# Kernel optimization log

Measured on AMD Instinct MI355X. Metric: run time of the kernel, lower is better.

## Reference

```python
import jax, jax.numpy as jnp
import numpy as np

HEADS, DIM_HEAD, DIM = 12, 64, 768
H = W = 32
N = H * W
B = 4


def _ln(x, g, b, eps=1e-5):
    mu = x.mean(-1, keepdims=True)
    var = ((x - mu) ** 2).mean(-1, keepdims=True)
    return (x - mu) / jnp.sqrt(var + eps) * g + b


def _get_epipolar(k, src_c2w, target_c2w, h=H, w=W):
    # Faithful port of Epipolar_Attention.get_epipolar, without the (hw*hw,3) repeat
    # materialization (uses broadcasting for the pairwise cross product instead).
    b = k.shape[0]
    Wf = h * 16.0 / 9.0
    k = k.astype(jnp.float32)
    k = k.at[:, 0, :].multiply(Wf).at[:, 1, :].multiply(float(h))
    k = k.at[:, 0, 2].set(h / 2.0).at[:, 1, 2].set(h / 2.0)
    ii, jj = jnp.meshgrid(jnp.arange(h), jnp.arange(w), indexing='ij')
    # after the torch column swap: (col, row, 1)
    coords = jnp.stack([jj.ravel(), ii.ravel(), jnp.ones(h * w, jnp.int32)], axis=1).astype(jnp.float32)  # [hw,3]
    k3 = k[:, :3, :3]
    src_r, src_t = src_c2w[:, :3, :3].astype(jnp.float32), src_c2w[:, :3, 3].astype(jnp.float32)
    tgt_r, tgt_t = target_c2w[:, :3, :3].astype(jnp.float32), target_c2w[:, :3, 3].astype(jnp.float32)
    tgt_rinv = jnp.linalg.inv(tgt_r)
    fx, fy = k3[:, 0, 0][:, None], k3[:, 1, 1][:, None]
    cx, cy = k3[:, 0, 2][:, None], k3[:, 1, 2][:, None]
    nc = jnp.stack([(coords[None, :, 0] - cx) / fx,
                    (coords[None, :, 1] - cy) / fy,
                    jnp.broadcast_to(coords[None, :, 2], (b, h * w))], axis=-1)  # [b,hw,3]
    p3w = jnp.einsum('bij,bnj->bni', src_r, nc) + src_t[:, None]
    p2 = jnp.einsum('bij,bnj->bni', tgt_rinv, p3w) - tgt_t[:, None]  # target_w2c_t = -target_c2w_t
    pij_un = jnp.einsum('bij,bnj->bni', k3, p2)                      # [b,hw,3]
    pij = pij_un / (pij_un[..., -1:] + 1e-6)
    o2 = jnp.einsum('bij,bj->bi', tgt_rinv, src_t) - tgt_t           # origin projected
    oij = jnp.einsum('bij,bj->bi', k3, o2)
    oij = oij / oij[..., -1:]
    oi_to_pi = pij - oij[:, None]                # [b,hw,3]
    oi_to_coord = coords[None] - oij[:, None]    # [b,hw,3]
    cr = jnp.cross(oi_to_pi[:, :, None, :], oi_to_coord[:, None, :, :])  # [b,hw,hw,3]
    area = jnp.sqrt((cr * cr).sum(-1))
    vlen = jnp.sqrt((oi_to_pi * oi_to_pi).sum(-1))[:, :, None]
    dist = area / vlen
    dw = 1.0 - jax.nn.sigmoid(50.0 * (dist - 0.5))
    row_max = dw.max(-1, keepdims=True)
    return jnp.where(row_max < 0.5, 1.0, dw)     # rows with max<0.5 are set to all-ones


def setup_inputs():
    key = jax.random.key(0)
    ks = jax.random.split(key, 16)
    s = 0.02
    x = jax.random.normal(ks[0], (B, N, DIM), jnp.float32)
    src_encode = jax.random.normal(ks[1], (B, N, DIM), jnp.float32)
    intrinsic = (jnp.zeros((B, 4, 4), jnp.float32)
                 .at[:, 0, 0].set(1.0).at[:, 1, 1].set(1.0)
                 .at[:, 0, 2].set(0.5).at[:, 1, 2].set(0.5)
                 .at[:, 2, 2].set(1.0).at[:, 3, 3].set(1.0))
    R = jnp.eye(3, dtype=jnp.float32) + 0.1 * jax.random.normal(ks[2], (2, B, 3, 3), jnp.float32)
    t = 0.5 * jax.random.normal(ks[3], (2, B, 3), jnp.float32)
    c2w = (jnp.zeros((2, B, 4, 4), jnp.float32)
           .at[:, :, :3, :3].set(R).at[:, :, :3, 3].set(t).at[:, :, 3, 3].set(1.0))
    hd = HEADS * DIM_HEAD
    w_ = lambda k_, shp: s * jax.random.normal(k_, shp, jnp.float32)
    return dict(
        x=x, src_encode=src_encode, intrinsic=intrinsic, c2w=c2w,
        lnq_g=jnp.ones(DIM), lnq_b=jnp.zeros(DIM), Wq=w_(ks[4], (DIM, hd)), bq=jnp.zeros(hd),
        lnk_g=jnp.ones(DIM), lnk_b=jnp.zeros(DIM), Wk=w_(ks[5], (DIM, hd)), bk=jnp.zeros(hd),
        lnv_g=jnp.ones(DIM), lnv_b=jnp.zeros(DIM), Wv=w_(ks[6], (DIM, hd)), bv=jnp.zeros(hd),
        Wp=w_(ks[7], (hd, DIM)), bp=jnp.zeros(DIM),
        pre_g=jnp.ones(DIM), pre_b=jnp.zeros(DIM),
        W1=w_(ks[8], (DIM, 2 * DIM)), b1=jnp.zeros(2 * DIM),
        W2=w_(ks[9], (2 * DIM, DIM)), b2=jnp.zeros(DIM),
        post_g=jnp.ones(DIM), post_b=jnp.zeros(DIM))


def reference(x, src_encode, intrinsic, c2w, lnq_g, lnq_b, Wq, bq, lnk_g, lnk_b, Wk, bk,
              lnv_g, lnv_b, Wv, bv, Wp, bp, pre_g, pre_b, W1, b1, W2, b2, post_g, post_b):
    b, n, _ = x.shape
    scale = DIM_HEAD ** -0.5
    split = lambda t_: t_.reshape(b, n, HEADS, DIM_HEAD).transpose(0, 2, 1, 3)  # [b,m,n,d]
    q = split(_ln(x, lnq_g, lnq_b) @ Wq + bq)
    k = split(_ln(src_encode, lnk_g, lnk_b) @ Wk + bk)
    v = split(_ln(src_encode, lnv_g, lnv_b) @ Wv + bv)
    scores = scale * jnp.einsum('bmqd,bmkd->bmqk', q, k)
    e1 = _get_epipolar(intrinsic, c2w[1], c2w[0])                    # do_epipolar
    e2 = jnp.swapaxes(_get_epipolar(intrinsic, c2w[0], c2w[1]), 1, 2)  # bidirectional (transposed)
    wmap = e1 * e2                                                   # [b,n,n], shared across heads
    att = jax.nn.softmax(scores * wmap[:, None], axis=-1)
    a = jnp.einsum('bmqk,bmkd->bmqd', att, v).transpose(0, 2, 1, 3).reshape(b, n, HEADS * DIM_HEAD)
    z = _ln(a @ Wp + bp, pre_g, pre_b)
    z = z + (jax.nn.gelu(z @ W1 + b1, approximate=False) @ W2 + b2)  # torch nn.GELU = exact erf
    z = _ln(z, post_g, post_b)
    wm_full = jnp.broadcast_to(wmap[:, None], (b, HEADS, n, n)).reshape(b * HEADS, n, n)
    return z, wm_full
```

## Files before the change

kernel.cpp:

```cpp
#include <hip/hip_runtime.h>
#include <hip/hip_bf16.h>

typedef unsigned short u16;
typedef __attribute__((ext_vector_type(4))) unsigned short u16x4;
typedef __attribute__((ext_vector_type(8))) unsigned short u16x8;
typedef __attribute__((ext_vector_type(8))) short s16x8;
typedef __attribute__((ext_vector_type(4))) float f32x4;

#define HEADS 12
#define NSEQ 1024
#define DIMM 768
#define DHEAD 64

__device__ __forceinline__ float b2f(u16 h) {
  union { unsigned u; float f; } v; v.u = ((unsigned)h) << 16; return v.f;
}
__device__ __forceinline__ u16 f2b(float f) {
  union { float f; unsigned u; } v; v.f = f;
  unsigned r = v.u + 0x7fffu + ((v.u >> 16) & 1u);
  return (u16)(r >> 16);
}
__device__ __forceinline__ void gl_lds16(const u16* g, u16* l) {
  __builtin_amdgcn_global_load_lds(
      (const __attribute__((address_space(1))) void*)g,
      (__attribute__((address_space(3))) void*)l, 16, 0, 0);
}

template<bool GELU, bool RESID, bool VTOUT>
__device__ __forceinline__ void gemm64(
    const u16* __restrict__ A, const u16* __restrict__ BT,
    const float* __restrict__ bias, const u16* __restrict__ resid,
    const float* __restrict__ rg, const float* __restrict__ rb,
    u16* __restrict__ C, int K, int lda, int ldb, int ldc,
    int m0, int n0, u16* As, u16* Bs, u16* __restrict__ vt)
{
  const int tid = threadIdx.x;
  const int lane = tid & 63;
  const int wv = tid >> 6;
  const int wm0 = (wv >> 1) * 32;
  const int wn0 = (wv & 1) * 32;
  const int l15 = lane & 15;
  const int quad = lane >> 4;
  const int srow = wv * 8 + (lane >> 3);
  const int schunk = lane & 7;
  const int scol = (schunk ^ (srow & 7)) * 8;

  f32x4 acc[2][2];
  #pragma unroll
  for (int i = 0; i < 2; ++i)
    #pragma unroll
    for (int j = 0; j < 2; ++j)
      acc[i][j] = {0.f, 0.f, 0.f, 0.f};

  const u16* Ab = A + (long)(m0 + srow) * lda + scol;
  const u16* Bb = BT + (long)(n0 + srow) * ldb + scol;

  auto issue = [&](int buf, int kk) {
    #pragma unroll
    for (int s = 0; s < 2; ++s) {
      gl_lds16(Ab + kk + (long)s * 32 * lda, As + buf * 4096 + s * 2048 + wv * 512);
      gl_lds16(Bb + kk + (long)s * 32 * ldb, Bs + buf * 4096 + s * 2048 + wv * 512);
    }
  };

  const int NK = K >> 6;
  issue(0, 0);
  issue(1, 64);

  int cur = 0;
  for (int i = 0; i < NK; ++i) {
    if (i + 1 < NK) asm volatile("s_waitcnt vmcnt(4)" ::: "memory");
    else            asm volatile("s_waitcnt vmcnt(0)" ::: "memory");
    __builtin_amdgcn_s_barrier();
    __builtin_amdgcn_sched_barrier(0);
    if (i + 2 < NK) {
      int nb = cur + 2; if (nb >= 3) nb -= 3;
      issue(nb, (i + 2) * 64);
    }
    const u16* Ac = As + cur * 4096;
    const u16* Bc = Bs + cur * 4096;
    #pragma unroll
    for (int kk = 0; kk < 2; ++kk) {
      s16x8 af[2], bfr[2];
      #pragma unroll
      for (int i2 = 0; i2 < 2; ++i2)
        af[i2] = *(const s16x8*)&Ac[(wm0 + i2 * 16 + l15) * 64 +
                                    (((kk * 4 + quad) ^ (l15 & 7)) * 8)];
      #pragma unroll
      for (int j = 0; j < 2; ++j)
        bfr[j] = *(const s16x8*)&Bc[(wn0 + j * 16 + l15) * 64 +
                                    (((kk * 4 + quad) ^ (l15 & 7)) * 8)];
      #pragma unroll
      for (int i2 = 0; i2 < 2; ++i2)
        #pragma unroll
        for (int j = 0; j < 2; ++j)
          acc[i2][j] = __builtin_amdgcn_mfma_f32_16x16x32_bf16(af[i2], bfr[j], acc[i2][j], 0, 0, 0);
    }
    ++cur; if (cur == 3) cur = 0;
  }

  if (VTOUT) {
    __syncthreads();
    u16* shp = As;
    const int b = m0 >> 10;
    const int nloc = m0 & 1023;
    const int fb0 = n0 - 768;
    #pragma unroll
    for (int j = 0; j < 2; ++j) {
      const float bvv = bias[n0 + wn0 + j * 16 + l15];
      #pragma unroll
      for (int i = 0; i < 2; ++i)
        #pragma unroll
        for (int v = 0; v < 4; ++v)
          shp[(wm0 + i * 16 + quad * 4 + v) * 72 + (wn0 + j * 16 + l15)] =
              f2b(acc[i][j][v] + bvv);
    }
    __syncthreads();
    const int f = tid >> 2;
    const int nb = (tid & 3) * 16;
    u16x8 o0, o1;
    #pragma unroll
    for (int nn = 0; nn < 8; ++nn) {
      o0[nn] = shp[(nb + nn) * 72 + f];
      o1[nn] = shp[(nb + 8 + nn) * 72 + f];
    }
    u16* dst = vt + ((long)(b * 768 + fb0 + f)) * NSEQ + nloc + nb;
    *(u16x8*)&dst[0] = o0;
    *(u16x8*)&dst[8] = o1;
    return;
  }

  #pragma unroll
  for (int i = 0; i < 2; ++i)
    #pragma unroll
    for (int j = 0; j < 2; ++j) {
      const int col = n0 + wn0 + j * 16 + l15;
      const float bvv = bias[col];
      #pragma unroll
      for (int v = 0; v < 4; ++v) {
        const int row = m0 + wm0 + i * 16 + quad * 4 + v;
        float val = acc[i][j][v] + bvv;
        if (GELU) val = 0.5f * val * (1.0f + erff(val * 0.70710678118654752440f));
        if (RESID) val += b2f(resid[(long)row * ldc + col]) * rg[col] + rb[col];
        C[(long)row * ldc + col] = f2b(val);
      }
    }
}

template<bool GELU, bool RESID>
__global__ __launch_bounds__(256)
void gemm_one(const u16* __restrict__ A, const u16* __restrict__ BT,
              const float* __restrict__ bias, const u16* __restrict__ resid,
              const float* __restrict__ rg, const float* __restrict__ rb,
              u16* __restrict__ C, int K, int lda, int ldb, int ldc)
{
  __shared__ u16 As[12288], Bs[12288];
  gemm64<GELU, RESID, false>(A, BT, bias, resid, rg, rb, C, K, lda, ldb, ldc,
                             blockIdx.x * 64, blockIdx.y * 64, As, Bs, nullptr);
}

__device__ __forceinline__ float dwval(f32x4 U, float ox, float oy, float oz, int m)
{
  const float cx = (float)(m & 31) - ox;
  const float cy = (float)(m >> 5) - oy;
  const float cz = 1.0f - oz;
  const float crx = U.y * cz - U.z * cy;
  const float cry = U.z * cx - U.x * cz;
  const float crz = U.x * cy - U.y * cx;
  const float area = sqrtf(crx * crx + cry * cry + crz * crz);
  const float dist = area / U.w;
  const float t = 50.0f * (dist - 0.5f);
  return 1.0f - 1.0f / (1.0f + __expf(-t));
}

#define PREP_T0 13824
#define PREP_T1 14016
#define PREP_T2 22208
#define PREP_T3 30400

__global__ __launch_bounds__(256)
void prep2(const float* w0, const float* w1, const float* w2,
           const float* w3, const float* w4, const float* w5,
           const float* gq, const float* gk, const float* gv, const float* gp,
           u16* d0, u16* d12, u16* d3, u16* d4, u16* d5,
           const float* bq, const float* bk, const float* bv, const float* b1,
           const float* lnqb, const float* lnkb, const float* lnvb, const float* preb,
           float* obq, float* obkv, float* ob1,
           const float* intr, const float* c2w,
           float* u4, float* oijb, float* flags,
           const float* nx, const float* nsrc, u16* onx, u16* onsrc)
{
  const int bid = blockIdx.x;
  const int tid = threadIdx.x;

  if (bid < PREP_T0) {
    __shared__ u16 t[32][36];
    const int z = bid / 2304;
    const int rem = bid - z * 2304;
    const int bx = rem % 48, by = rem / 48;
    const float* src; const float* g; u16* dst; int R, C; float sc = 1.0f;
    switch (z) {
      case 0: src = w0; g = gq; dst = d0;  R = 768;  C = 768;  sc = 0.125f; break;
      case 1: src = w1; g = gk; dst = d12; R = 768;  C = 768;  break;
      case 2: src = w2; g = gv; dst = d12 + 768 * 768; R = 768; C = 768; break;
      case 3: src = w3; g = nullptr; dst = d3; R = 768;  C = 768;  break;
      case 4: src = w4; g = gp; dst = d4; R = 768;  C = 1536; break;
      default: src = w5; g = nullptr; dst = d5; R = 1536; C = 768; break;
    }
    const int c0 = bx * 32;
    const int r0 = by * 32;
    if (c0 >= C || r0 >= R) return;
    const int i = tid >> 3;
    const int j4 = (tid & 7) * 4;
    const float rs = (g ? g[r0 + i] : 1.0f) * sc;
    #pragma unroll
    for (int jj = 0; jj < 4; ++jj)
      t[i][j4 + jj] = f2b(src[(long)(r0 + i) * C + c0 + j4 + jj] * rs);
    __syncthreads();
    u16x4 ov;
    #pragma unroll
    for (int jj = 0; jj < 4; ++jj) ov[jj] = t[j4 + jj][i];
    *(u16x4*)&dst[(long)(c0 + i) * R + r0 + j4] = ov;
    return;
  }

  if (bid < PREP_T1) {
    __shared__ float red[8][32];
    const int idx = bid - PREP_T0;
    const int y = idx / 48;
    const int bx = idx % 48;
    const float* W; const float* bln; const float* bw; float* out;
    int C; float sc = 1.0f;
    switch (y) {
      case 0: W = w0; bln = lnqb; bw = bq; out = obq;        C = 768;  sc = 0.125f; break;
      case 1: W = w1; bln = lnkb; bw = bk; out = obkv;       C = 768;  break;
      case 2: W = w2; bln = lnvb; bw = bv; out = obkv + 768; C = 768;  break;
      default: W = w4; bln = preb; bw = b1; out = ob1;       C = 1536; break;
    }
    const int c0 = bx * 32;
    if (c0 >= C) return;
    const int cl = tid & 31;
    const int rg = tid >> 5;
    const int c = c0 + cl;
    float s = 0.f;
    for (int r = rg * 96; r < rg * 96 + 96; ++r)
      s += bln[r] * W[(long)r * C + c];
    red[rg][cl] = s;
    __syncthreads();
    if (rg == 0) {
      float tot = bw[c];
      #pragma unroll
      for (int k = 0; k < 8; ++k) tot += red[k][cl];
      out[c] = tot * sc;
    }
    return;
  }

  if (bid < PREP_T2) {
    __shared__ float S[40];
    __shared__ float redf[8];
    const int rowid = bid - PREP_T1;
    const int db = rowid >> 10;
    const int n = rowid & 1023;
    const int d = db >> 2, b = db & 3;
    if (tid == 0) {
      const int sidx = (d == 0) ? 1 : 0;
      const int tidx = 1 - sidx;
      float k3[9], sr[9], st[3], tr[9], tt[3];
      const float Wf = 32.0f * 16.0f / 9.0f;
      for (int j = 0; j < 3; ++j) {
        k3[j]     = intr[(b * 4 + 0) * 4 + j] * Wf;
        k3[3 + j] = intr[(b * 4 + 1) * 4 + j] * 32.0f;
        k3[6 + j] = intr[(b * 4 + 2) * 4 + j];
      }
      k3[2] = 16.0f; k3[5] = 16.0f;
      for (int i = 0; i < 3; ++i) {
        for (int j = 0; j < 3; ++j) {
          sr[i * 3 + j] = c2w[((sidx * 4 + b) * 4 + i) * 4 + j];
          tr[i * 3 + j] = c2w[((tidx * 4 + b) * 4 + i) * 4 + j];
        }
        st[i] = c2w[((sidx * 4 + b) * 4 + i) * 4 + 3];
        tt[i] = c2w[((tidx * 4 + b) * 4 + i) * 4 + 3];
      }
      double a = tr[0], bb_ = tr[1], c = tr[2];
      double dd2 = tr[3], e = tr[4], f = tr[5];
      double g2 = tr[6], h2 = tr[7], i2 = tr[8];
      double det = a * (e * i2 - f * h2) - bb_ * (dd2 * i2 - f * g2) + c * (dd2 * h2 - e * g2);
      double inv[9] = {
        (e * i2 - f * h2), (c * h2 - bb_ * i2), (bb_ * f - c * e),
        (f * g2 - dd2 * i2), (a * i2 - c * g2), (c * dd2 - a * f),
        (dd2 * h2 - e * g2), (bb_ * g2 - a * h2), (a * e - bb_ * dd2)
      };
      float tri[9];
      for (int t2 = 0; t2 < 9; ++t2) tri[t2] = (float)(inv[t2] / det);
      float o2[3], oij[3];
      for (int i3 = 0; i3 < 3; ++i3)
        o2[i3] = tri[i3 * 3] * st[0] + tri[i3 * 3 + 1] * st[1] + tri[i3 * 3 + 2] * st[2] - tt[i3];
      for (int i3 = 0; i3 < 3; ++i3)
        oij[i3] = k3[i3 * 3] * o2[0] + k3[i3 * 3 + 1] * o2[1] + k3[i3 * 3 + 2] * o2[2];
      const float ozf = oij[2];
      oij[0] = oij[0] / ozf; oij[1] = oij[1] / ozf; oij[2] = ozf / ozf;
      if (n == 0) {
        oijb[db * 4 + 0] = oij[0]; oijb[db * 4 + 1] = oij[1];
        oijb[db * 4 + 2] = oij[2]; oijb[db * 4 + 3] = 0.f;
      }
      const float ncx = ((float)(n & 31) - k3[2]) / k3[0];
      const float ncy = ((float)(n >> 5) - k3[5]) / k3[4];
      const float p0 = sr[0] * ncx + sr[1] * ncy + sr[2] + st[0];
      const float p1 = sr[3] * ncx + sr[4] * ncy + sr[5] + st[1];
      const float p2 = sr[6] * ncx + sr[7] * ncy + sr[8] + st[2];
      const float q0 = tri[0] * p0 + tri[1] * p1 + tri[2] * p2 - tt[0];
      const float q1 = tri[3] * p0 + tri[4] * p1 + tri[5] * p2 - tt[1];
      const float q2 = tri[6] * p0 + tri[7] * p1 + tri[8] * p2 - tt[2];
      const float ww0 = k3[0] * q0 + k3[1] * q1 + k3[2] * q2;
      const float ww1 = k3[3] * q0 + k3[4] * q1 + k3[5] * q2;
      const float ww2 = k3[6] * q0 + k3[7] * q1 + k3[8] * q2;
      const float pz = ww2 + 1e-6f;
      const float ux = ww0 / pz - oij[0];
      const float uy = ww1 / pz - oij[1];
      const float uz = ww2 / pz - oij[2];
      const float vlen = sqrtf(ux * ux + uy * uy + uz * uz);
      f32x4 uo = {ux, uy, uz, vlen};
      *(f32x4*)&u4[(long)rowid * 4] = uo;
      S[33] = oij[0]; S[34] = oij[1]; S[35] = oij[2];
      S[36] = ux; S[37] = uy; S[38] = uz; S[39] = vlen;
    }
    __syncthreads();
    const f32x4 U = {S[36], S[37], S[38], S[39]};
    const float ox = S[33], oy = S[34], oz = S[35];
    float mx = -1e30f;
    #pragma unroll
    for (int i = 0; i < 4; ++i)
      mx = fmaxf(mx, dwval(U, ox, oy, oz, tid + i * 256));
    #pragma unroll
    for (int off = 32; off; off >>= 1) mx = fmaxf(mx, __shfl_down(mx, off));
    const int lane = tid & 63, wid = tid >> 6;
    if (!lane) redf[wid] = mx;
    __syncthreads();
    if (!tid) {
      const float m4 = fmaxf(fmaxf(redf[0], redf[1]), fmaxf(redf[2], redf[3]));
      flags[rowid] = (m4 < 0.5f) ? 1.0f : 0.0f;
    }
    return;
  }

  {
    __shared__ float s1[8], s2[8];
    const int r = bid - PREP_T2;
    const float* p = ((r < 4096) ? nx : nsrc) + (long)(r & 4095) * DIMM;
    u16* o = ((r < 4096) ? onx : onsrc) + (long)(r & 4095) * DIMM;
    float v0 = p[tid], v1 = p[tid + 256], v2 = p[tid + 512];
    float s = v0 + v1 + v2;
    #pragma unroll
    for (int off = 32; off; off >>= 1) s += __shfl_down(s, off);
    const int lane = tid & 63, wid = tid >> 6;
    if (!lane) s1[wid] = s;
    __syncthreads();
    if (!tid) s1[4] = s1[0] + s1[1] + s1[2] + s1[3];
    __syncthreads();
    const float mu = s1[4] / 768.0f;
    float d0 = v0 - mu, d1 = v1 - mu, d2 = v2 - mu;
    float sq = d0 * d0 + d1 * d1 + d2 * d2;
    #pragma unroll
    for (int off = 32; off; off >>= 1) sq += __shfl_down(sq, off);
    if (!lane) s2[wid] = sq;
    __syncthreads();
    if (!tid) s2[4] = s2[0] + s2[1] + s2[2] + s2[3];
    __syncthreads();
    const float rstd = 1.0f / sqrtf(s2[4] / 768.0f + 1e-5f);
    o[tid]       = f2b(d0 * rstd);
    o[tid + 256] = f2b(d1 * rstd);
    o[tid + 512] = f2b(d2 * rstd);
  }
}

__global__ __launch_bounds__(256)
void stageB(const u16* __restrict__ nx, const u16* __restrict__ ns,
            const u16* __restrict__ qT, const u16* __restrict__ kvT,
            const float* __restrict__ bqf, const float* __restrict__ bkvf,
            u16* __restrict__ qb, u16* __restrict__ kvb, u16* __restrict__ vT,
            const float* __restrict__ u4, const float* __restrict__ oijb,
            const float* __restrict__ flags,
            u16* __restrict__ wm, float* __restrict__ wm_full)
{
  __shared__ __align__(16) u16 sh[24576];
  const int bid = blockIdx.x;
  const int tid = threadIdx.x;

  if (bid < 2304) {
    u16* As = sh;
    u16* Bs = sh + 12288;
    const int z = bid / 768;
    const int idx = bid - z * 768;
    const int x = idx & 63;
    const int y = idx >> 6;
    if (z == 0)
      gemm64<false, false, false>(nx, qT, bqf, nullptr, nullptr, nullptr, qb,
                                  768, 768, 768, 768,
                                  x * 64, y * 64, As, Bs, nullptr);
    else if (z == 1)
      gemm64<false, false, false>(ns, kvT, bkvf, nullptr, nullptr, nullptr, kvb,
                                  768, 768, 768, 1536,
                                  x * 64, y * 64, As, Bs, nullptr);
    else
      gemm64<false, false, true>(ns, kvT, bkvf, nullptr, nullptr, nullptr, nullptr,
                                 768, 768, 768, 1536,
                                 x * 64, 768 + y * 64, As, Bs, vT);
    return;
  }

  const int id = bid - 2304;
  const int qx = id & 31;
  const int ky = (id >> 5) & 31;
  const int b = id >> 10;
  const int q0 = qx * 32;
  const int k0 = ky * 32;
  const int i = tid >> 3;
  const int j4 = (tid & 7) * 4;

  f32x4* U2s = (f32x4*)sh;
  float* f2s = (float*)(sh + 256);
  float* f1s = (float*)(sh + 320);
  if (tid < 32) {
    U2s[tid] = *(const f32x4*)&u4[((long)(4 + b) * 1024 + k0 + tid) * 4];
    f2s[tid] = flags[(4 + b) * 1024 + k0 + tid];
    f1s[tid] = flags[b * 1024 + q0 + tid];
  }
  __syncthreads();

  const int q = q0 + i;
  const f32x4 U1 = *(const f32x4*)&u4[((long)b * 1024 + q) * 4];
  const float o1x = oijb[b * 4 + 0], o1y = oijb[b * 4 + 1], o1z = oijb[b * 4 + 2];
  const float o2x = oijb[(4 + b) * 4 + 0], o2y = oijb[(4 + b) * 4 + 1], o2z = oijb[(4 + b) * 4 + 2];
  const bool fl1 = f1s[i] > 0.5f;

  u16x4 pk;
  f32x4 wf;
  #pragma unroll
  for (int jj = 0; jj < 4; ++jj) {
    const int k = k0 + j4 + jj;
    const float e1 = fl1 ? 1.0f : dwval(U1, o1x, o1y, o1z, k);
    const float e2 = (f2s[j4 + jj] > 0.5f) ? 1.0f : dwval(U2s[j4 + jj], o2x, o2y, o2z, q);
    const float w = e1 * e2;
    wf[jj] = w;
    pk[jj] = f2b(w);
  }
  *(u16x4*)&wm[((long)b * 1024 + q0 + i) * 1024 + k0 + j4] = pk;
  #pragma unroll
  for (int h = 0; h < HEADS; ++h)
    *(f32x4*)&wm_full[((long)(b * HEADS + h) * 1024 + q0 + i) * 1024 + k0 + j4] = wf;
}

__global__ __launch_bounds__(256, 3)
void fattn(const u16* __restrict__ qb, const u16* __restrict__ kvb,
           const u16* __restrict__ vT, const u16* __restrict__ wm,
           u16* __restrict__ outA)
{
  __shared__ u16 Qs[2 * 64 * 32];
  __shared__ u16 Ks[2][2 * 64 * 32];
  __shared__ u16 Vs[2][2 * 64 * 32];
  __shared__ u16 Ps[64][72];

  const int bh = blockIdx.y;
  const int b = bh / HEADS, h = bh - b * HEADS;
  const int q0 = blockIdx.x * 64;
  const int tid = threadIdx.x;
  const int lane = tid & 63;
  const int wv = tid >> 6;
  const int l15 = lane & 15;
  const int quad = lane >> 4;
  const int srow = lane >> 2;
  const int sscol = ((lane & 3) ^ (srow & 3)) * 8;
  const int rch = (quad ^ (l15 & 3)) * 8;

  const u16* Qg = qb + ((long)b * NSEQ + q0) * DIMM + h * DHEAD;
  const u16* Kg = kvb + (long)b * NSEQ * 1536 + h * DHEAD;
  const u16* Vg = vT + (long)bh * DHEAD * NSEQ;
  const u16* Wg = wm + ((long)b * NSEQ + q0) * NSEQ;

  #pragma unroll
  for (int h2 = 0; h2 < 2; ++h2) {
    gl_lds16(Qg + (long)(wv * 16 + srow) * DIMM + h2 * 32 + sscol,
             Qs + (h2 * 64 + wv * 16) * 32);
    gl_lds16(Kg + (long)(wv * 16 + srow) * 1536 + h2 * 32 + sscol,
             Ks[0] + (h2 * 64 + wv * 16) * 32);
    gl_lds16(Vg + (long)(wv * 16 + srow) * NSEQ + h2 * 32 + sscol,
             Vs[0] + (h2 * 64 + wv * 16) * 32);
  }

  f32x4 Sacc[4], Oacc[4];
  float mrow[4], lrow[4];
  #pragma unroll
  for (int j = 0; j < 4; ++j) {
    Oacc[j] = {0.f, 0.f, 0.f, 0.f};
    mrow[j] = -3.0e38f;
    lrow[j] = 0.f;
  }
  s16x8 qf[2];

  int cur = 0;
  for (int kt = 0; kt < 16; ++kt) {
    __syncthreads();
    if (kt < 15) {
      const int nxt = cur ^ 1;
      #pragma unroll
      for (int h2 = 0; h2 < 2; ++h2) {
        gl_lds16(Kg + (long)((kt + 1) * 64 + wv * 16 + srow) * 1536 + h2 * 32 + sscol,
                 Ks[nxt] + (h2 * 64 + wv * 16) * 32);
        gl_lds16(Vg + (long)(wv * 16 + srow) * NSEQ + (kt + 1) * 64 + h2 * 32 + sscol,
                 Vs[nxt] + (h2 * 64 + wv * 16) * 32);
      }
    }

    if (kt == 0) {
      qf[0] = *(const s16x8*)&Qs[(0 * 64 + wv * 16 + l15) * 32 + rch];
      qf[1] = *(const s16x8*)&Qs[(1 * 64 + wv * 16 + l15) * 32 + rch];
    }

    float wr[4][4];
    #pragma unroll
    for (int j = 0; j < 4; ++j)
      #pragma unroll
      for (int v = 0; v < 4; ++v)
        wr[j][v] = b2f(Wg[(long)(wv * 16 + quad * 4 + v) * NSEQ + kt * 64 + j * 16 + l15]);

    #pragma unroll
    for (int j = 0; j < 4; ++j) Sacc[j] = {0.f, 0.f, 0.f, 0.f};
    #pragma unroll
    for (int j = 0; j < 4; ++j)
      #pragma unroll
      for (int h2 = 0; h2 < 2; ++h2) {
        s16x8 kf = *(const s16x8*)&Ks[cur][(h2 * 64 + j * 16 + l15) * 32 + rch];
        Sacc[j] = __builtin_amdgcn_mfma_f32_16x16x32_bf16(qf[h2], kf, Sacc[j], 0, 0, 0);
      }

    #pragma unroll
    for (int j = 0; j < 4; ++j)
      #pragma unroll
      for (int v = 0; v < 4; ++v)
        Sacc[j][v] *= wr[j][v];
    #pragma unroll
    for (int v = 0; v < 4; ++v) {
      float tm = fmaxf(fmaxf(Sacc[0][v], Sacc[1][v]), fmaxf(Sacc[2][v], Sacc[3][v]));
      tm = fmaxf(tm, __shfl_xor(tm, 1));
      tm = fmaxf(tm, __shfl_xor(tm, 2));
      tm = fmaxf(tm, __shfl_xor(tm, 4));
      tm = fmaxf(tm, __shfl_xor(tm, 8));
      const float mnew = fmaxf(mrow[v], tm);
      const float al = __expf(mrow[v] - mnew);
      float rs = 0.f;
      #pragma unroll
      for (int j = 0; j < 4; ++j) {
        const float e = __expf(Sacc[j][v] - mnew);
        Sacc[j][v] = e;
        rs += e;
      }
      rs += __shfl_xor(rs, 1);
      rs += __shfl_xor(rs, 2);
      rs += __shfl_xor(rs, 4);
      rs += __shfl_xor(rs, 8);
      lrow[v] = lrow[v] * al + rs;
      mrow[v] = mnew;
      #pragma unroll
      for (int jn = 0; jn < 4; ++jn) Oacc[jn][v] *= al;
    }
    #pragma unroll
    for (int j = 0; j < 4; ++j)
      #pragma unroll
      for (int v = 0; v < 4; ++v)
        Ps[wv * 16 + quad * 4 + v][j * 16 + l15] = f2b(Sacc[j][v]);

    #pragma unroll
    for (int h2 = 0; h2 < 2; ++h2) {
      s16x8 af = *(const s16x8*)&Ps[wv * 16 + l15][h2 * 32 + quad * 8];
      #pragma unroll
      for (int jn = 0; jn < 4; ++jn) {
        s16x8 vf = *(const s16x8*)&Vs[cur][(h2 * 64 + jn * 16 + l15) * 32 + rch];
        Oacc[jn] = __builtin_amdgcn_mfma_f32_16x16x32_bf16(af, vf, Oacc[jn], 0, 0, 0);
      }
    }
    cur ^= 1;
  }

  #pragma unroll
  for (int v = 0; v < 4; ++v) {
    const int row = q0 + wv * 16 + quad * 4 + v;
    const float inv = 1.0f / lrow[v];
    #pragma unroll
    for (int jn = 0; jn < 4; ++jn)
      outA[((long)(b * NSEQ + row)) * DIMM + h * DHEAD + jn * 16 + l15] =
          f2b(Oacc[jn][v] * inv);
  }
}

__global__ __launch_bounds__(256)
void norm_k(const u16* __restrict__ in, u16* __restrict__ out)
{
  const long base = (long)blockIdx.x * DIMM;
  const int tid = threadIdx.x;
  __shared__ float s1[8], s2[8];
  const u16* p = in + base;
  float v0 = b2f(p[tid]), v1 = b2f(p[tid + 256]), v2 = b2f(p[tid + 512]);
  float s = v0 + v1 + v2;
  #pragma unroll
  for (int off = 32; off; off >>= 1) s += __shfl_down(s, off);
  const int lane = tid & 63, wid = tid >> 6;
  if (!lane) s1[wid] = s;
  __syncthreads();
  if (!tid) s1[4] = s1[0] + s1[1] + s1[2] + s1[3];
  __syncthreads();
  const float mu = s1[4] / 768.0f;
  float d0 = v0 - mu, d1 = v1 - mu, d2 = v2 - mu;
  float sq = d0 * d0 + d1 * d1 + d2 * d2;
  #pragma unroll
  for (int off = 32; off; off >>= 1) sq += __shfl_down(sq, off);
  if (!lane) s2[wid] = sq;
  __syncthreads();
  if (!tid) s2[4] = s2[0] + s2[1] + s2[2] + s2[3];
  __syncthreads();
  const float rstd = 1.0f / sqrtf(s2[4] / 768.0f + 1e-5f);
  u16* o = out + base;
  o[tid]       = f2b(d0 * rstd);
  o[tid + 256] = f2b(d1 * rstd);
  o[tid + 512] = f2b(d2 * rstd);
}

__global__ __launch_bounds__(256)
void ln_final(const u16* __restrict__ in, const float* __restrict__ g,
              const float* __restrict__ bb, float* __restrict__ out)
{
  const long base = (long)blockIdx.x * DIMM;
  const int tid = threadIdx.x;
  __shared__ float s1[8], s2[8];
  const u16* p = in + base;
  float v0 = b2f(p[tid]), v1 = b2f(p[tid + 256]), v2 = b2f(p[tid + 512]);
  float s = v0 + v1 + v2;
  #pragma unroll
  for (int off = 32; off; off >>= 1) s += __shfl_down(s, off);
  const int lane = tid & 63, wid = tid >> 6;
  if (!lane) s1[wid] = s;
  __syncthreads();
  if (!tid) s1[4] = s1[0] + s1[1] + s1[2] + s1[3];
  __syncthreads();
  const float mu = s1[4] / 768.0f;
  float d0 = v0 - mu, d1 = v1 - mu, d2 = v2 - mu;
  float sq = d0 * d0 + d1 * d1 + d2 * d2;
  #pragma unroll
  for (int off = 32; off; off >>= 1) sq += __shfl_down(sq, off);
  if (!lane) s2[wid] = sq;
  __syncthreads();
  if (!tid) s2[4] = s2[0] + s2[1] + s2[2] + s2[3];
  __syncthreads();
  const float rstd = 1.0f / sqrtf(s2[4] / 768.0f + 1e-5f);
  float* o = out + base;
  o[tid]       = d0 * rstd * g[tid]       + bb[tid];
  o[tid + 256] = d1 * rstd * g[tid + 256] + bb[tid + 256];
  o[tid + 512] = d2 * rstd * g[tid + 512] + bb[tid + 512];
}

extern "C" void kernel_launch(void* const* d_in, const int* in_sizes, int n_in,
                              void* d_out, int out_size, void* d_ws, size_t ws_size,
                              hipStream_t stream)
{
  (void)in_sizes; (void)n_in; (void)out_size; (void)ws_size;
  const float* x     = (const float*)d_in[0];
  const float* src   = (const float*)d_in[1];
  const float* intr  = (const float*)d_in[2];
  const float* c2w   = (const float*)d_in[3];
  const float* lnq_g = (const float*)d_in[4];
  const float* lnq_b = (const float*)d_in[5];
  const float* Wq    = (const float*)d_in[6];
  const float* bq    = (const float*)d_in[7];
  const float* lnk_g = (const float*)d_in[8];
  const float* lnk_b = (const float*)d_in[9];
  const float* Wk    = (const float*)d_in[10];
  const float* bk    = (const float*)d_in[11];
  const float* lnv_g = (const float*)d_in[12];
  const float* lnv_b = (const float*)d_in[13];
  const float* Wv    = (const float*)d_in[14];
  const float* bv    = (const float*)d_in[15];
  const float* Wp    = (const float*)d_in[16];
  const float* bp    = (const float*)d_in[17];
  const float* pre_g = (const float*)d_in[18];
  const float* pre_b = (const float*)d_in[19];
  const float* W1    = (const float*)d_in[20];
  const float* b1    = (const float*)d_in[21];
  const float* W2    = (const float*)d_in[22];
  const float* b2    = (const float*)d_in[23];
  const float* post_g= (const float*)d_in[24];
  const float* post_b= (const float*)d_in[25];

  char* ws = (char*)d_ws;
  size_t off = 0;
  auto alloc = [&](size_t bytes) -> char* {
    char* p = ws + off;
    off = (off + bytes + 255) & ~(size_t)255;
    return p;
  };
  const size_t SEQD = (size_t)4096 * 768 * 2;

  u16* WqT  = (u16*)alloc(768 * 768 * 2);
  u16* WkvT = (u16*)alloc((size_t)1536 * 768 * 2);
  u16* WpT  = (u16*)alloc(768 * 768 * 2);
  u16* W1T  = (u16*)alloc(768 * 1536 * 2);
  u16* W2T  = (u16*)alloc(1536 * 768 * 2);
  float* bqf  = (float*)alloc(768 * 4);
  float* bkvf = (float*)alloc(1536 * 4);
  float* b1f  = (float*)alloc(1536 * 4);
  char* pool = alloc(6 * SEQD);
  float* u4   = (float*)alloc(8 * 1024 * 4 * 4);
  float* oijb = (float*)alloc(8 * 4 * 4);
  u16* wmapb  = (u16*)alloc((size_t)4 * 1024 * 1024 * 2);
  float* flagb = (float*)alloc(8 * 1024 * 4);

  u16* S0 = (u16*)pool;
  u16* S1 = (u16*)(pool + SEQD);
  u16* S2 = (u16*)(pool + 2 * SEQD);
  u16* S3 = (u16*)(pool + 3 * SEQD);
  u16* S5 = (u16*)(pool + 5 * SEQD);

  float* out_z  = (float*)d_out;
  float* out_wm = (float*)d_out + (size_t)4 * 1024 * 768;

  prep2<<<PREP_T3, 256, 0, stream>>>(
      Wq, Wk, Wv, Wp, W1, W2, lnq_g, lnk_g, lnv_g, pre_g,
      WqT, WkvT, WpT, W1T, W2T,
      bq, bk, bv, b1, lnq_b, lnk_b, lnv_b, pre_b,
      bqf, bkvf, b1f,
      intr, c2w, u4, oijb, flagb,
      x, src, S0, S1);

  stageB<<<6400, 256, 0, stream>>>(
      S0, S1, WqT, WkvT, bqf, bkvf, S2, S3, S5,
      u4, oijb, flagb, wmapb, out_wm);

  fattn<<<dim3(16, 48), 256, 0, stream>>>(S2, S3, S5, wmapb, S0);

  gemm_one<false, false><<<dim3(64, 12), 256, 0, stream>>>(
      S0, WpT, bp, nullptr, nullptr, nullptr, S1, 768, 768, 768, 768);

  norm_k<<<4096, 256, 0, stream>>>(S1, S2);

  gemm_one<true, false><<<dim3(64, 24), 256, 0, stream>>>(
      S2, W1T, b1f, nullptr, nullptr, nullptr, S3, 768, 768, 768, 1536);

  gemm_one<false, true><<<dim3(64, 12), 256, 0, stream>>>(
      S3, W2T, b2, S2, pre_g, pre_b, S5, 1536, 1536, 1536, 768);

  ln_final<<<4096, 256, 0, stream>>>(S5, post_g, post_b, out_z);
}
```

Measured before the change: 461.2 us.

## Pre-swizzle epipolar weight map into MFMA fragment order and add XCD block swizzling

StageB now writes the bf16 weight map in a per-tile layout matching each fattn thread's MFMA accumulator fragment, so fattn reads it with two 16-byte vector loads instead of sixteen strided scalar loads. The GEMM, stageB and fattn blocks are remapped so neighbouring tiles land on the same XCD for better L2 reuse, and the LDS bank swizzle in fattn is changed. The cost is scattered 2-byte stores when stageB writes the weight map.

```diff
diff --git a/kernel.cpp b/kernel.cpp
--- a/kernel.cpp
+++ b/kernel.cpp
@@ -155,8 +155,13 @@
               u16* __restrict__ C, int K, int lda, int ldb, int ldc)
 {
   __shared__ u16 As[12288], Bs[12288];
+  const int total = gridDim.x * gridDim.y;
+  const int fid = blockIdx.y * gridDim.x + blockIdx.x;
+  const int swz = (fid & 7) * (total >> 3) + (fid >> 3);
+  const int x = swz & 63;
+  const int y = swz >> 6;
   gemm64<GELU, RESID, false>(A, BT, bias, resid, rg, rb, C, K, lda, ldb, ldc,
-                             blockIdx.x * 64, blockIdx.y * 64, As, Bs, nullptr);
+                             x * 64, y * 64, As, Bs, nullptr);
 }
 
 __device__ __forceinline__ float dwval(f32x4 U, float ox, float oy, float oz, int m)
@@ -381,7 +386,7 @@
             u16* __restrict__ qb, u16* __restrict__ kvb, u16* __restrict__ vT,
             const float* __restrict__ u4, const float* __restrict__ oijb,
             const float* __restrict__ flags,
-            u16* __restrict__ wm, float* __restrict__ wm_full)
+            u16* __restrict__ wm2, float* __restrict__ wm_full)
 {
   __shared__ __align__(16) u16 sh[24576];
   const int bid = blockIdx.x;
@@ -390,8 +395,9 @@
   if (bid < 2304) {
     u16* As = sh;
     u16* Bs = sh + 12288;
-    const int z = bid / 768;
-    const int idx = bid - z * 768;
+    const int swz = (bid & 7) * 288 + (bid >> 3);
+    const int z = swz / 768;
+    const int idx = swz - z * 768;
     const int x = idx & 63;
     const int y = idx >> 6;
     if (z == 0)
@@ -434,7 +440,12 @@
   const float o2x = oijb[(4 + b) * 4 + 0], o2y = oijb[(4 + b) * 4 + 1], o2z = oijb[(4 + b) * 4 + 2];
   const bool fl1 = f1s[i] > 0.5f;
 
-  u16x4 pk;
+  const int Q = q >> 6;
+  const int qr = q & 63;
+  const int wv2 = qr >> 4, qd = (qr >> 2) & 3, v2 = qr & 3;
+  const int kt = (k0 + j4) >> 6;
+  u16* w2base = wm2 + ((((long)b * 16 + Q) * 16 + kt) * 256) * 16;
+
   f32x4 wf;
   #pragma unroll
   for (int jj = 0; jj < 4; ++jj) {
@@ -443,9 +454,11 @@
     const float e2 = (f2s[j4 + jj] > 0.5f) ? 1.0f : dwval(U2s[j4 + jj], o2x, o2y, o2z, q);
     const float w = e1 * e2;
     wf[jj] = w;
-    pk[jj] = f2b(w);
-  }
-  *(u16x4*)&wm[((long)b * 1024 + q0 + i) * 1024 + k0 + j4] = pk;
+    const int kc = k & 63;
+    const int j2 = kc >> 4, l2 = kc & 15;
+    const int ftid = wv2 * 64 + qd * 16 + l2;
+    w2base[ftid * 16 + j2 * 4 + v2] = f2b(w);
+  }
   #pragma unroll
   for (int h = 0; h < HEADS; ++h)
     *(f32x4*)&wm_full[((long)(b * HEADS + h) * 1024 + q0 + i) * 1024 + k0 + j4] = wf;
@@ -453,7 +466,7 @@
 
 __global__ __launch_bounds__(256, 3)
 void fattn(const u16* __restrict__ qb, const u16* __restrict__ kvb,
-           const u16* __restrict__ vT, const u16* __restrict__ wm,
+           const u16* __restrict__ vT, const u16* __restrict__ wm2,
            u16* __restrict__ outA)
 {
   __shared__ u16 Qs[2 * 64 * 32];
@@ -461,22 +474,27 @@
   __shared__ u16 Vs[2][2 * 64 * 32];
   __shared__ u16 Ps[64][72];
 
-  const int bh = blockIdx.y;
-  const int b = bh / HEADS, h = bh - b * HEADS;
-  const int q0 = blockIdx.x * 64;
+  const int fid = blockIdx.x;
+  const int swz = (fid & 7) * 96 + (fid >> 3);
+  const int b = swz / 192;
+  const int r = swz - b * 192;
+  const int x = r / 12;
+  const int h = r - x * 12;
+  const int bh = b * HEADS + h;
+  const int q0 = x * 64;
   const int tid = threadIdx.x;
   const int lane = tid & 63;
   const int wv = tid >> 6;
   const int l15 = lane & 15;
   const int quad = lane >> 4;
   const int srow = lane >> 2;
-  const int sscol = ((lane & 3) ^ (srow & 3)) * 8;
-  const int rch = (quad ^ (l15 & 3)) * 8;
+  const int sscol = ((lane & 3) ^ ((lane >> 3) & 3)) * 8;
+  const int rch = (quad ^ ((l15 >> 1) & 3)) * 8;
 
   const u16* Qg = qb + ((long)b * NSEQ + q0) * DIMM + h * DHEAD;
   const u16* Kg = kvb + (long)b * NSEQ * 1536 + h * DHEAD;
   const u16* Vg = vT + (long)bh * DHEAD * NSEQ;
-  const u16* Wg = wm + ((long)b * NSEQ + q0) * NSEQ;
+  const u16* W2 = wm2 + ((((long)b * 16 + x) * 16) * 256) * 16;
 
   #pragma unroll
   for (int h2 = 0; h2 < 2; ++h2) {
@@ -517,12 +535,16 @@
       qf[1] = *(const s16x8*)&Qs[(1 * 64 + wv * 16 + l15) * 32 + rch];
     }
 
+    const u16x8 wa = *(const u16x8*)&W2[((long)kt * 256 + tid) * 16];
+    const u16x8 wb = *(const u16x8*)&W2[((long)kt * 256 + tid) * 16 + 8];
     float wr[4][4];
     #pragma unroll
-    for (int j = 0; j < 4; ++j)
-      #pragma unroll
-      for (int v = 0; v < 4; ++v)
-        wr[j][v] = b2f(Wg[(long)(wv * 16 + quad * 4 + v) * NSEQ + kt * 64 + j * 16 + l15]);
+    for (int v = 0; v < 4; ++v) {
+      wr[0][v] = b2f(wa[v]);
+      wr[1][v] = b2f(wa[4 + v]);
+      wr[2][v] = b2f(wb[v]);
+      wr[3][v] = b2f(wb[4 + v]);
+    }
 
     #pragma unroll
     for (int j = 0; j < 4; ++j) Sacc[j] = {0.f, 0.f, 0.f, 0.f};
@@ -710,7 +732,7 @@
   char* pool = alloc(6 * SEQD);
   float* u4   = (float*)alloc(8 * 1024 * 4 * 4);
   float* oijb = (float*)alloc(8 * 4 * 4);
-  u16* wmapb  = (u16*)alloc((size_t)4 * 1024 * 1024 * 2);
+  u16* wm2b   = (u16*)alloc((size_t)4 * 1024 * 1024 * 2);
   float* flagb = (float*)alloc(8 * 1024 * 4);
 
   u16* S0 = (u16*)pool;
@@ -732,9 +754,9 @@
 
   stageB<<<6400, 256, 0, stream>>>(
       S0, S1, WqT, WkvT, bqf, bkvf, S2, S3, S5,
-      u4, oijb, flagb, wmapb, out_wm);
-
-  fattn<<<dim3(16, 48), 256, 0, stream>>>(S2, S3, S5, wmapb, S0);
+      u4, oijb, flagb, wm2b, out_wm);
+
+  fattn<<<768, 256, 0, stream>>>(S2, S3, S5, wm2b, S0);
 
   gemm_one<false, false><<<dim3(64, 12), 256, 0, stream>>>(
       S0, WpT, bp, nullptr, nullptr, nullptr, S1, 768, 768, 768, 768);
```

Result: no change. 467.1 us (+1.3%).
